# Optimization experiments

Hardware: AMD Instinct MI355X
Metric: run time of the kernel (lower is better)

## Reference

```python
import jax, jax.numpy as jnp
import numpy as np

B, S, D = 2, 2048, 1024
H = 16
DK = D // H


def setup_inputs() -> dict:
    key = jax.random.key(0)
    ks = jax.random.split(key, 5)
    std = np.sqrt(2.0 / (D + D))
    x = jax.random.normal(ks[0], (B, S, D), dtype=jnp.float32)
    wq = jax.random.normal(ks[1], (D, D), dtype=jnp.float32) * std
    wk = jax.random.normal(ks[2], (D, D), dtype=jnp.float32) * std
    wv = jax.random.normal(ks[3], (D, D), dtype=jnp.float32) * std
    wo = jax.random.normal(ks[4], (D, D), dtype=jnp.float32) * std
    return {"x": x, "wq": wq, "wk": wk, "wv": wv, "wo": wo}


def reference(x, wq, wk, wv, wo):
    # Linear: y = x @ W.T  (weight stored as [d_out, d_in])
    q = jnp.einsum("bsd,ed->bse", x, wq)
    k = jnp.einsum("bsd,ed->bse", x, wk)
    v = jnp.einsum("bsd,ed->bse", x, wv)
    # split heads: [B, S, H*DK] -> [B, H, S, DK]
    q = q.reshape(B, S, H, DK).transpose(0, 2, 1, 3)
    k = k.reshape(B, S, H, DK).transpose(0, 2, 1, 3)
    v = v.reshape(B, S, H, DK).transpose(0, 2, 1, 3)
    scale = 1.0 / jnp.sqrt(jnp.asarray(DK, dtype=x.dtype))
    scores = jnp.einsum("bhqd,bhkd->bhqk", q, k) * scale  # [B,H,S,S]
    causal = jnp.tril(jnp.ones((S, S), dtype=bool))
    scores = jnp.where(causal, scores, -jnp.inf)
    attn = jax.nn.softmax(scores, axis=-1)
    out = jnp.einsum("bhqk,bhkd->bhqd", attn, v)  # [B,H,S,DK]
    out = out.transpose(0, 2, 1, 3).reshape(B, S, D)
    return jnp.einsum("bsd,ed->bse", out, wo)
```

## Files before the change

kernel.cpp:

```cpp
#include <hip/hip_runtime.h>
#include <hip/hip_bf16.h>
#include <cstdint>

#define B_ 2
#define S_ 2048
#define D_ 1024
#define H_ 16
#define DK_ 64

#define LOG2E_S 0.18033688f

typedef __attribute__((ext_vector_type(8))) short bf16x8;
typedef __attribute__((ext_vector_type(4))) float f32x4;

__device__ __forceinline__ unsigned short f2bf(float f) {
  unsigned u = __float_as_uint(f);
  u = (u + 0x7FFFu + ((u >> 16) & 1u)) >> 16;
  return (unsigned short)u;
}

__device__ __forceinline__ unsigned short f2bf_hw(float f) {
  __hip_bfloat16 h = __float2bfloat16(f);
  return *reinterpret_cast<unsigned short*>(&h);
}

typedef __attribute__((address_space(1))) void gv_t;
typedef __attribute__((address_space(3))) void lv_t;
__device__ __forceinline__ void gl16(const void* g, void* l) {
  __builtin_amdgcn_global_load_lds((gv_t*)g, (lv_t*)l, 16, 0, 0);
}

__device__ __forceinline__ void stage8w(const unsigned short* gbase, size_t ldg,
                                        unsigned short* lds, int wave, int lane) {
  const int lr = lane >> 3;
  const int col8 = (lane & 7) ^ lr;
  gl16(gbase + (size_t)(wave * 8 + lr) * ldg + col8 * 8, lds + wave * 512);
}

__device__ __forceinline__ bf16x8 rdswz(const unsigned short* lds, int row, int col) {
  return *(const bf16x8*)&lds[row * 64 + (col ^ ((row & 7) << 3))];
}

__global__ void cvt_all_kernel(const float* __restrict__ x,
                               const float* __restrict__ w0, const float* __restrict__ w1,
                               const float* __restrict__ w2, const float* __restrict__ w3,
                               unsigned short* __restrict__ xo,
                               unsigned short* __restrict__ o0, unsigned short* __restrict__ o1,
                               unsigned short* __restrict__ o2, unsigned short* __restrict__ o3) {
  const int NX4 = 1 << 20;
  const int TOT = 1 << 21;
  for (int i = blockIdx.x * blockDim.x + threadIdx.x; i < TOT; i += gridDim.x * blockDim.x) {
    const float* in;
    unsigned short* out;
    int off;
    if (i < NX4) {
      in = x; out = xo; off = i;
    } else {
      int j = i - NX4;
      int mat = j >> 18;
      off = j & ((1 << 18) - 1);
      in = (mat == 0) ? w0 : (mat == 1) ? w1 : (mat == 2) ? w2 : w3;
      out = (mat == 0) ? o0 : (mat == 1) ? o1 : (mat == 2) ? o2 : o3;
    }
    const float4 v = reinterpret_cast<const float4*>(in)[off];
    ushort4 o;
    o.x = f2bf(v.x); o.y = f2bf(v.y); o.z = f2bf(v.z); o.w = f2bf(v.w);
    reinterpret_cast<ushort4*>(out)[off] = o;
  }
}

#define BM 128
#define BK 64

template <typename OutT, bool TV2, int BNv, bool SCALEQ>
__global__ __launch_bounds__(256) void gemm_bt(
    const unsigned short* __restrict__ A,
    const unsigned short* __restrict__ B0, const unsigned short* __restrict__ B1,
    const unsigned short* __restrict__ B2,
    OutT* __restrict__ C0, OutT* __restrict__ C1, OutT* __restrict__ C2,
    int M, int N, int K) {
  constexpr int NFRAG = BNv / 32;
  __shared__ unsigned short lA[BM * BK];
  __shared__ unsigned short lB[BNv * BK];
  const int tid = threadIdx.x;
  const int wave = tid >> 6, lane = tid & 63;
  const int l16 = lane & 15, lqq = lane >> 4;
  const int wr = wave >> 1, wc = wave & 1;
  const int lr = lane >> 3;
  const int col8 = ((lane & 7) ^ lr) * 8;

  const int tilesPerMat = N / BNv;
  const int bx = blockIdx.x;
  const int mat = bx / tilesPerMat;
  const int n0 = (bx % tilesPerMat) * BNv;
  const unsigned short* Bm = (mat == 0) ? B0 : (mat == 1) ? B1 : B2;
  OutT* C = (mat == 0) ? C0 : (mat == 1) ? C1 : C2;
  const int m0 = blockIdx.y * BM;

  f32x4 acc[4][NFRAG] = {};

  for (int k0 = 0; k0 < K; k0 += BK) {
    __syncthreads();
#pragma unroll
    for (int c = wave; c < 16; c += 4)
      gl16(A + (size_t)(m0 + c * 8 + lr) * K + k0 + col8, &lA[c * 512]);
#pragma unroll
    for (int c = wave; c < BNv / 8; c += 4)
      gl16(Bm + (size_t)(n0 + c * 8 + lr) * K + k0 + col8, &lB[c * 512]);
    __syncthreads();
#pragma unroll
    for (int kk = 0; kk < BK / 32; ++kk) {
      bf16x8 af[4], bfr[NFRAG];
#pragma unroll
      for (int m = 0; m < 4; ++m)
        af[m] = rdswz(lA, wr * 64 + m * 16 + l16, kk * 32 + lqq * 8);
#pragma unroll
      for (int n = 0; n < NFRAG; ++n)
        bfr[n] = rdswz(lB, wc * (BNv / 2) + n * 16 + l16, kk * 32 + lqq * 8);
      __builtin_amdgcn_s_setprio(1);
#pragma unroll
      for (int m = 0; m < 4; ++m)
#pragma unroll
        for (int n = 0; n < NFRAG; ++n)
          acc[m][n] = __builtin_amdgcn_mfma_f32_16x16x32_bf16(af[m], bfr[n], acc[m][n], 0, 0, 0);
      __builtin_amdgcn_s_setprio(0);
    }
  }

  if (TV2 && mat == 2) {
    unsigned short* Vt = (unsigned short*)C;
#pragma unroll
    for (int m = 0; m < 4; ++m)
#pragma unroll
      for (int n = 0; n < NFRAG; ++n) {
        int r0 = m0 + wr * 64 + m * 16 + lqq * 4;
        int cidx = n0 + wc * (BNv / 2) + n * 16 + l16;
        int bb = r0 >> 11, s = r0 & 2047;
        int h = cidx >> 6, dv = cidx & 63;
        ushort4 o;
        o.x = f2bf(acc[m][n][0]); o.y = f2bf(acc[m][n][1]);
        o.z = f2bf(acc[m][n][2]); o.w = f2bf(acc[m][n][3]);
        *(ushort4*)(Vt + ((size_t)((bb * H_ + h) * DK_ + dv)) * S_ + s) = o;
      }
  } else {
    const float cscale = (SCALEQ && mat == 0) ? LOG2E_S : 1.0f;
#pragma unroll
    for (int m = 0; m < 4; ++m)
#pragma unroll
      for (int n = 0; n < NFRAG; ++n)
#pragma unroll
        for (int j = 0; j < 4; ++j) {
          int r = m0 + wr * 64 + m * 16 + lqq * 4 + j;
          int cidx = n0 + wc * (BNv / 2) + n * 16 + l16;
          float v = acc[m][n][j] * cscale;
          if constexpr (sizeof(OutT) == 4) C[(size_t)r * N + cidx] = v;
          else C[(size_t)r * N + cidx] = f2bf(v);
        }
  }
}

__global__ __launch_bounds__(512) void attn_kernel(
    const unsigned short* __restrict__ Qg, const unsigned short* __restrict__ Kg,
    const unsigned short* __restrict__ Vtg, unsigned short* __restrict__ Og) {
  __shared__ unsigned short sK[2][64 * 64];
  __shared__ unsigned short sVt[2][64 * 64];
  __shared__ unsigned short sP[8][2][16 * 64];
  const int tid = threadIdx.x, wave = tid >> 6, lane = tid & 63;
  const int side = wave >> 2, wq = wave & 3;
  const int l16 = lane & 15, lq = lane >> 4;
  const int id = blockIdx.x;
  const int bh = (id & 7) * 4 + ((id >> 3) & 3);
  const int g = (id >> 5) & 7;
  const int i = (id < 256) ? (15 - g) : g;
  const int b = bh >> 4, h = bh & 15;
  const int qtA = 2 * i, qtB = 2 * i + 1;
  const int qt_s = side ? qtB : qtA;
  const int NT = i + 1;
  const size_t tokbase = (size_t)b * S_ * D_ + h * DK_;
  const unsigned short* VtB = Vtg + (size_t)(b * H_ + h) * DK_ * S_;
  unsigned short (*sPw)[16 * 64] = sP[wave];

  stage8w(Kg + tokbase, D_, sK[0], wave, lane);
  stage8w(Kg + tokbase + (size_t)64 * D_, D_, sK[1], wave, lane);
  stage8w(VtB, S_, sVt[0], wave, lane);
  stage8w(VtB + 64, S_, sVt[1], wave, lane);
  const unsigned short* qrow = Qg + tokbase + (size_t)(qt_s * 64 + wq * 16 + l16) * D_;
  bf16x8 aq0 = *(const bf16x8*)(qrow + lq * 8);
  bf16x8 aq1 = *(const bf16x8*)(qrow + 32 + lq * 8);
  __syncthreads();

  const float THR2 = 11.5416f;
  const short ONE_BF = 0x3F80;
  const bf16x8 vones = {ONE_BF, ONE_BF, ONE_BF, ONE_BF, ONE_BF, ONE_BF, ONE_BF, ONE_BF};
  float m_run[4] = {-1e30f, -1e30f, -1e30f, -1e30f};
  f32x4 sum_acc = {};
  f32x4 o_acc[4] = {};

#pragma unroll 1
  for (int kt = 0; kt < NT; ++kt) {
    const bool last = (kt == NT - 1);
    float p[8][4];

#pragma unroll
    for (int sub = 0; sub < 2; ++sub) {
      const bool skip = (sub == 1) && (side == 0) && last;
      if (!skip) {
        __builtin_amdgcn_s_setprio(1);
#pragma unroll
        for (int nb = 0; nb < 4; ++nb) {
          bf16x8 bk0 = rdswz(sK[sub], nb * 16 + l16, lq * 8);
          bf16x8 bk1 = rdswz(sK[sub], nb * 16 + l16, 32 + lq * 8);
          f32x4 a = {};
          a = __builtin_amdgcn_mfma_f32_16x16x32_bf16(aq0, bk0, a, 0, 0, 0);
          a = __builtin_amdgcn_mfma_f32_16x16x32_bf16(aq1, bk1, a, 0, 0, 0);
#pragma unroll
          for (int j = 0; j < 4; ++j) p[sub * 4 + nb][j] = a[j];
        }
        __builtin_amdgcn_s_setprio(0);
      } else {
#pragma unroll
        for (int nb = 0; nb < 4; ++nb)
#pragma unroll
          for (int j = 0; j < 4; ++j) p[sub * 4 + nb][j] = -1e30f;
      }
    }

    __syncthreads();
    if (kt + 1 < NT) {
      stage8w(Kg + tokbase + (size_t)((kt + 1) * 128) * D_, D_, sK[0], wave, lane);
      stage8w(Kg + tokbase + (size_t)((kt + 1) * 128 + 64) * D_, D_, sK[1], wave, lane);
    }

    if (last) {
      if (side == 0) {
#pragma unroll
        for (int nb = 0; nb < 4; ++nb)
#pragma unroll
          for (int j = 0; j < 4; ++j) {
            int kidx = nb * 16 + l16;
            int qidx = wq * 16 + lq * 4 + j;
            if (kidx > qidx) p[nb][j] = -1e30f;
          }
      } else {
#pragma unroll
        for (int nb = 0; nb < 4; ++nb)
#pragma unroll
          for (int j = 0; j < 4; ++j) {
            int kidx = nb * 16 + l16;
            int qidx = wq * 16 + lq * 4 + j;
            if (kidx > qidx) p[4 + nb][j] = -1e30f;
          }
      }
    }

    float pmax[4];
    bool ok = true;
#pragma unroll
    for (int j = 0; j < 4; ++j) {
      float r = p[0][j];
#pragma unroll
      for (int nbb = 1; nbb < 8; ++nbb) r = fmaxf(r, p[nbb][j]);
      pmax[j] = r;
      ok = ok && (r <= m_run[j] + THR2);
    }
    if (!__all((int)ok)) {
#pragma unroll
      for (int j = 0; j < 4; ++j) {
        float r = pmax[j];
#pragma unroll
        for (int d = 1; d < 16; d <<= 1) r = fmaxf(r, __shfl_xor(r, d));
        float mn = fmaxf(m_run[j], r);
        float alpha = exp2f(m_run[j] - mn);
        m_run[j] = mn;
        sum_acc[j] *= alpha;
#pragma unroll
        for (int nb = 0; nb < 4; ++nb) o_acc[nb][j] *= alpha;
      }
    }
#pragma unroll
    for (int j = 0; j < 4; ++j) {
      const int rw = lq * 4 + j;
#pragma unroll
      for (int nbb = 0; nbb < 8; ++nbb) {
        float e = exp2f(p[nbb][j] - m_run[j]);
        sPw[nbb >> 2][rw * 64 + (((nbb & 3) * 16 + l16) ^ ((rw & 7) << 3))] = f2bf_hw(e);
      }
    }

    __builtin_amdgcn_s_setprio(1);
#pragma unroll
    for (int sub = 0; sub < 2; ++sub)
#pragma unroll
      for (int kk = 0; kk < 2; ++kk) {
        bf16x8 ap = rdswz(sPw[sub], l16, kk * 32 + lq * 8);
        sum_acc = __builtin_amdgcn_mfma_f32_16x16x32_bf16(ap, vones, sum_acc, 0, 0, 0);
#pragma unroll
        for (int nb = 0; nb < 4; ++nb) {
          bf16x8 bv = rdswz(sVt[sub], nb * 16 + l16, kk * 32 + lq * 8);
          o_acc[nb] = __builtin_amdgcn_mfma_f32_16x16x32_bf16(ap, bv, o_acc[nb], 0, 0, 0);
        }
      }
    __builtin_amdgcn_s_setprio(0);

    __syncthreads();
    if (kt + 1 < NT) {
      stage8w(VtB + (kt + 1) * 128, S_, sVt[0], wave, lane);
      stage8w(VtB + (kt + 1) * 128 + 64, S_, sVt[1], wave, lane);
    }
  }

#pragma unroll
  for (int j = 0; j < 4; ++j) {
    float inv = 1.f / sum_acc[j];
#pragma unroll
    for (int nb = 0; nb < 4; ++nb) {
      int r = qt_s * 64 + wq * 16 + lq * 4 + j;
      Og[tokbase + (size_t)r * D_ + nb * 16 + l16] = f2bf(o_acc[nb][j] * inv);
    }
  }
}

extern "C" void kernel_launch(void* const* d_in, const int* in_sizes, int n_in,
                              void* d_out, int out_size, void* d_ws, size_t ws_size,
                              hipStream_t stream) {
  const float* x = (const float*)d_in[0];
  const float* wq = (const float*)d_in[1];
  const float* wk = (const float*)d_in[2];
  const float* wv = (const float*)d_in[3];
  const float* wo = (const float*)d_in[4];
  float* out = (float*)d_out;

  char* ws = (char*)d_ws;
  const size_t MB = 1024 * 1024;
  unsigned short* xb  = (unsigned short*)(ws + 0);
  unsigned short* wqb = (unsigned short*)(ws + 8 * MB);
  unsigned short* wkb = (unsigned short*)(ws + 10 * MB);
  unsigned short* wvb = (unsigned short*)(ws + 12 * MB);
  unsigned short* wob = (unsigned short*)(ws + 14 * MB);
  unsigned short* Qb  = (unsigned short*)(ws + 16 * MB);
  unsigned short* Kb  = (unsigned short*)(ws + 24 * MB);
  unsigned short* Vtb = (unsigned short*)(ws + 32 * MB);
  unsigned short* AOb = (unsigned short*)(ws + 40 * MB);

  const int M = B_ * S_;
  const int N = D_, K = D_;

  cvt_all_kernel<<<dim3(2048), 256, 0, stream>>>(
      x, wq, wk, wv, wo, xb, wqb, wkb, wvb, wob);

  gemm_bt<unsigned short, true, 128, true><<<dim3(3 * (N / 128), M / BM), 256, 0, stream>>>(
      xb, wqb, wkb, wvb, Qb, Kb, Vtb, M, N, K);

  attn_kernel<<<dim3(512), 512, 0, stream>>>(Qb, Kb, Vtb, AOb);

  gemm_bt<float, false, 64, false><<<dim3(N / 64, M / BM), 256, 0, stream>>>(
      AOb, wob, wob, wob, out, out, out, M, N, K);
}
```

Before: 105.1 us.

## Split long causal attention rows across two KV chunks with a combine pass

Query-tile groups from index 10 upward are split into two blocks, each covering half of the KV range. Each writes unnormalized fp32 partial outputs plus running max and sum into workspace, and a new combine kernel merges them into the bf16 attention output. The aim is a shorter critical path and better load balance across CUs on the causal triangle. The P staging buffer is also halved by writing and consuming one 64-key sub-tile at a time, which cuts LDS use. The cost is an extra kernel launch and extra fp32 partial traffic, stored in workspace regions whose earlier contents are no longer needed.

```diff
diff --git a/kernel.cpp b/kernel.cpp
--- a/kernel.cpp
+++ b/kernel.cpp
@@ -9,6 +9,9 @@
 #define DK_ 64
 
 #define LOG2E_S 0.18033688f
+
+#define SPLIT_LO 10
+#define NPROWS 24576
 
 typedef __attribute__((ext_vector_type(8))) short bf16x8;
 typedef __attribute__((ext_vector_type(4))) float f32x4;
@@ -161,29 +164,36 @@
 
 __global__ __launch_bounds__(512) void attn_kernel(
     const unsigned short* __restrict__ Qg, const unsigned short* __restrict__ Kg,
-    const unsigned short* __restrict__ Vtg, unsigned short* __restrict__ Og) {
+    const unsigned short* __restrict__ Vtg, unsigned short* __restrict__ Og,
+    float* __restrict__ O0p, float* __restrict__ O1p, float* __restrict__ MSp) {
   __shared__ unsigned short sK[2][64 * 64];
   __shared__ unsigned short sVt[2][64 * 64];
-  __shared__ unsigned short sP[8][2][16 * 64];
+  __shared__ unsigned short sP[8][16 * 64];
   const int tid = threadIdx.x, wave = tid >> 6, lane = tid & 63;
   const int side = wave >> 2, wq = wave & 3;
   const int l16 = lane & 15, lq = lane >> 4;
   const int id = blockIdx.x;
-  const int bh = (id & 7) * 4 + ((id >> 3) & 3);
-  const int g = (id >> 5) & 7;
-  const int i = (id < 256) ? (15 - g) : g;
+  int u, ii, chunk;
+  if (id < 320)      { u = id;       ii = u >> 5;            chunk = -1; }
+  else if (id < 512) { u = id - 320; ii = SPLIT_LO + (u >> 5); chunk = 0; }
+  else               { u = id - 512; ii = SPLIT_LO + (u >> 5); chunk = 1; }
+  const int bh = (u & 7) * 4 + ((u >> 3) & 3);
   const int b = bh >> 4, h = bh & 15;
-  const int qtA = 2 * i, qtB = 2 * i + 1;
+  const int qtA = 2 * ii, qtB = 2 * ii + 1;
   const int qt_s = side ? qtB : qtA;
-  const int NT = i + 1;
+  const int NTf = ii + 1;
+  const int c0 = (NTf + 1) >> 1;
+  const int kt0 = (chunk == 1) ? c0 : 0;
+  const int ktN = (chunk == 0) ? c0 : NTf;
+  const bool hd = (chunk != 0);
   const size_t tokbase = (size_t)b * S_ * D_ + h * DK_;
   const unsigned short* VtB = Vtg + (size_t)(b * H_ + h) * DK_ * S_;
-  unsigned short (*sPw)[16 * 64] = sP[wave];
-
-  stage8w(Kg + tokbase, D_, sK[0], wave, lane);
-  stage8w(Kg + tokbase + (size_t)64 * D_, D_, sK[1], wave, lane);
-  stage8w(VtB, S_, sVt[0], wave, lane);
-  stage8w(VtB + 64, S_, sVt[1], wave, lane);
+  unsigned short* sPw = sP[wave];
+
+  stage8w(Kg + tokbase + (size_t)(kt0 * 128) * D_, D_, sK[0], wave, lane);
+  stage8w(Kg + tokbase + (size_t)(kt0 * 128 + 64) * D_, D_, sK[1], wave, lane);
+  stage8w(VtB + kt0 * 128, S_, sVt[0], wave, lane);
+  stage8w(VtB + kt0 * 128 + 64, S_, sVt[1], wave, lane);
   const unsigned short* qrow = Qg + tokbase + (size_t)(qt_s * 64 + wq * 16 + l16) * D_;
   bf16x8 aq0 = *(const bf16x8*)(qrow + lq * 8);
   bf16x8 aq1 = *(const bf16x8*)(qrow + 32 + lq * 8);
@@ -197,13 +207,13 @@
   f32x4 o_acc[4] = {};
 
 #pragma unroll 1
-  for (int kt = 0; kt < NT; ++kt) {
-    const bool last = (kt == NT - 1);
+  for (int kt = kt0; kt < ktN; ++kt) {
+    const bool last = (kt == ktN - 1);
     float p[8][4];
 
 #pragma unroll
     for (int sub = 0; sub < 2; ++sub) {
-      const bool skip = (sub == 1) && (side == 0) && last;
+      const bool skip = hd && (sub == 1) && (side == 0) && last;
       if (!skip) {
         __builtin_amdgcn_s_setprio(1);
 #pragma unroll
@@ -226,12 +236,12 @@
     }
 
     __syncthreads();
-    if (kt + 1 < NT) {
+    if (kt + 1 < ktN) {
       stage8w(Kg + tokbase + (size_t)((kt + 1) * 128) * D_, D_, sK[0], wave, lane);
       stage8w(Kg + tokbase + (size_t)((kt + 1) * 128 + 64) * D_, D_, sK[1], wave, lane);
     }
 
-    if (last) {
+    if (hd && last) {
       if (side == 0) {
 #pragma unroll
         for (int nb = 0; nb < 4; ++nb)
@@ -278,21 +288,24 @@
       }
     }
 #pragma unroll
-    for (int j = 0; j < 4; ++j) {
-      const int rw = lq * 4 + j;
-#pragma unroll
-      for (int nbb = 0; nbb < 8; ++nbb) {
-        float e = exp2f(p[nbb][j] - m_run[j]);
-        sPw[nbb >> 2][rw * 64 + (((nbb & 3) * 16 + l16) ^ ((rw & 7) << 3))] = f2bf_hw(e);
-      }
-    }
-
-    __builtin_amdgcn_s_setprio(1);
-#pragma unroll
-    for (int sub = 0; sub < 2; ++sub)
+    for (int j = 0; j < 4; ++j)
+#pragma unroll
+      for (int nbb = 0; nbb < 8; ++nbb)
+        p[nbb][j] = exp2f(p[nbb][j] - m_run[j]);
+
+#pragma unroll
+    for (int sub = 0; sub < 2; ++sub) {
+#pragma unroll
+      for (int j = 0; j < 4; ++j) {
+        const int rw = lq * 4 + j;
+#pragma unroll
+        for (int nb = 0; nb < 4; ++nb)
+          sPw[rw * 64 + (((nb * 16 + l16) ^ ((rw & 7) << 3)))] = f2bf_hw(p[sub * 4 + nb][j]);
+      }
+      __builtin_amdgcn_s_setprio(1);
 #pragma unroll
       for (int kk = 0; kk < 2; ++kk) {
-        bf16x8 ap = rdswz(sPw[sub], l16, kk * 32 + lq * 8);
+        bf16x8 ap = rdswz(sPw, l16, kk * 32 + lq * 8);
         sum_acc = __builtin_amdgcn_mfma_f32_16x16x32_bf16(ap, vones, sum_acc, 0, 0, 0);
 #pragma unroll
         for (int nb = 0; nb < 4; ++nb) {
@@ -300,23 +313,63 @@
           o_acc[nb] = __builtin_amdgcn_mfma_f32_16x16x32_bf16(ap, bv, o_acc[nb], 0, 0, 0);
         }
       }
-    __builtin_amdgcn_s_setprio(0);
+      __builtin_amdgcn_s_setprio(0);
+    }
 
     __syncthreads();
-    if (kt + 1 < NT) {
+    if (kt + 1 < ktN) {
       stage8w(VtB + (kt + 1) * 128, S_, sVt[0], wave, lane);
       stage8w(VtB + (kt + 1) * 128 + 64, S_, sVt[1], wave, lane);
     }
   }
 
-#pragma unroll
-  for (int j = 0; j < 4; ++j) {
-    float inv = 1.f / sum_acc[j];
-#pragma unroll
-    for (int nb = 0; nb < 4; ++nb) {
-      int r = qt_s * 64 + wq * 16 + lq * 4 + j;
-      Og[tokbase + (size_t)r * D_ + nb * 16 + l16] = f2bf(o_acc[nb][j] * inv);
-    }
+  if (chunk < 0) {
+#pragma unroll
+    for (int j = 0; j < 4; ++j) {
+      float inv = 1.f / sum_acc[j];
+#pragma unroll
+      for (int nb = 0; nb < 4; ++nb) {
+        int r = qt_s * 64 + wq * 16 + lq * 4 + j;
+        Og[tokbase + (size_t)r * D_ + nb * 16 + l16] = f2bf(o_acc[nb][j] * inv);
+      }
+    }
+  } else {
+    float* Op = chunk ? O1p : O0p;
+    const int prb = ((((ii - SPLIT_LO) * 32 + bh) * 2 + side) * 64) + wq * 16 + lq * 4;
+#pragma unroll
+    for (int j = 0; j < 4; ++j) {
+#pragma unroll
+      for (int nb = 0; nb < 4; ++nb)
+        Op[(size_t)(prb + j) * 64 + nb * 16 + l16] = o_acc[nb][j];
+      if (l16 == 0) {
+        MSp[((size_t)chunk * NPROWS + prb + j) * 2] = m_run[j];
+        MSp[((size_t)chunk * NPROWS + prb + j) * 2 + 1] = sum_acc[j];
+      }
+    }
+  }
+}
+
+__global__ __launch_bounds__(256) void combine_kernel(
+    const float* __restrict__ O0, const float* __restrict__ O1,
+    const float* __restrict__ MS, unsigned short* __restrict__ Og) {
+  int t = blockIdx.x * 256 + threadIdx.x;
+  int r = t >> 2, d0 = (t & 3) * 16;
+  int pi = r >> 12;
+  int rem = r & 4095;
+  int bh = rem >> 7, side = (rem >> 6) & 1, row = rem & 63;
+  int qt = 2 * (SPLIT_LO + pi) + side;
+  int b = bh >> 4, h = bh & 15;
+  float m0 = MS[(size_t)r * 2],            s0 = MS[(size_t)r * 2 + 1];
+  float m1 = MS[(size_t)(NPROWS + r) * 2], s1 = MS[(size_t)(NPROWS + r) * 2 + 1];
+  float m = fmaxf(m0, m1);
+  float a0 = exp2f(m0 - m), a1 = exp2f(m1 - m);
+  float inv = 1.f / (s0 * a0 + s1 * a1);
+  size_t obase = (size_t)b * S_ * D_ + h * DK_ + (size_t)(qt * 64 + row) * D_ + d0;
+  size_t pbase = (size_t)r * 64 + d0;
+#pragma unroll
+  for (int d = 0; d < 16; ++d) {
+    float o = (O0[pbase + d] * a0 + O1[pbase + d] * a1) * inv;
+    Og[obase + d] = f2bf(o);
   }
 }
 
@@ -341,6 +394,9 @@
   unsigned short* Kb  = (unsigned short*)(ws + 24 * MB);
   unsigned short* Vtb = (unsigned short*)(ws + 32 * MB);
   unsigned short* AOb = (unsigned short*)(ws + 40 * MB);
+  float* O0p = (float*)(ws + 0);
+  float* MSp = (float*)(ws + 6 * MB);
+  float* O1p = (float*)(ws + 8 * MB);
 
   const int M = B_ * S_;
   const int N = D_, K = D_;
@@ -351,7 +407,9 @@
   gemm_bt<unsigned short, true, 128, true><<<dim3(3 * (N / 128), M / BM), 256, 0, stream>>>(
       xb, wqb, wkb, wvb, Qb, Kb, Vtb, M, N, K);
 
-  attn_kernel<<<dim3(512), 512, 0, stream>>>(Qb, Kb, Vtb, AOb);
+  attn_kernel<<<dim3(704), 512, 0, stream>>>(Qb, Kb, Vtb, AOb, O0p, O1p, MSp);
+
+  combine_kernel<<<dim3(NPROWS * 4 / 256), 256, 0, stream>>>(O0p, O1p, MSp, AOb);
 
   gemm_bt<float, false, 64, false><<<dim3(N / 64, M / BM), 256, 0, stream>>>(
       AOb, wob, wob, wob, out, out, out, M, N, K);
```

Measured after the change: 115.5 us. +9.9%, slower.
